# Kernel tuning notes

Measured on AMD Instinct MI355X. Metric: run time of the kernel, lower is better.

## Reference

```python
import jax, jax.numpy as jnp
import numpy as np

# Static config (matches init_kwargs / docstring example)
SHAPES = ((100, 100), (50, 50), (25, 25), (13, 13))  # (H, W) per level
L, P, NH, HD, E, F = 4, 4, 8, 32, 256, 1024
NUM_LAYERS = 6
EPS = 1e-5
NUM_KEYS = sum(h * w for h, w in SHAPES)  # 13294


def _ln(x, g, b):
    m = jnp.mean(x, -1, keepdims=True)
    v = jnp.var(x, -1, keepdims=True)
    return (x - m) * jax.lax.rsqrt(v + EPS) * g + b


def _ms_deform_attn(value, loc, aw):
    # value: (B,N,NH,HD)  loc: (B,N,NH,L,P,2) normalized  aw: (B,N,NH,L,P)
    B, N = value.shape[:2]
    out = jnp.zeros((B, NH, N, HD), value.dtype)
    start = 0
    for lvl, (h, w) in enumerate(SHAPES):
        v = value[:, start:start + h * w].transpose(0, 2, 1, 3)  # (B,NH,hw,HD)
        start += h * w
        # grid_sample align_corners=False pixel coords
        x = loc[:, :, :, lvl, :, 0] * w - 0.5  # (B,N,NH,P)
        y = loc[:, :, :, lvl, :, 1] * h - 0.5
        x0 = jnp.floor(x); y0 = jnp.floor(y)
        lx = x - x0; ly = y - y0
        x0 = x0.astype(jnp.int32); y0 = y0.astype(jnp.int32)

        def gather(yi, xi):
            valid = ((xi >= 0) & (xi < w) & (yi >= 0) & (yi < h)).astype(value.dtype)
            idx = jnp.clip(yi, 0, h - 1) * w + jnp.clip(xi, 0, w - 1)  # (B,N,NH,P)
            idx = idx.transpose(0, 2, 1, 3).reshape(B, NH, N * P, 1)
            got = jnp.take_along_axis(v, idx, axis=2).reshape(B, NH, N, P, HD)
            return got * valid.transpose(0, 2, 1, 3)[..., None]

        def wgt(a):  # (B,N,NH,P) -> (B,NH,N,P,1)
            return a.transpose(0, 2, 1, 3)[..., None]

        samp = (gather(y0, x0) * wgt((1 - lx) * (1 - ly))
                + gather(y0, x0 + 1) * wgt(lx * (1 - ly))
                + gather(y0 + 1, x0) * wgt((1 - lx) * ly)
                + gather(y0 + 1, x0 + 1) * wgt(lx * ly))  # (B,NH,N,P,HD)
        out = out + jnp.sum(samp * wgt(aw[:, :, :, lvl]), axis=3)
    return out.transpose(0, 2, 1, 3).reshape(B, N, NH * HD)


def _layer(x, ref, Woff, boff, Waw, baw, Wv, bv, Wo, bo, ln1_g, ln1_b, Wf1, bf1, Wf2, bf2, ln2_g, ln2_b):
    B, N, _ = x.shape
    v = (x @ Wv + bv).reshape(B, N, NH, HD)
    off = (x @ Woff + boff).reshape(B, N, NH, L, P, 2)
    aw = jax.nn.softmax((x @ Waw + baw).reshape(B, N, NH, L * P), -1).reshape(B, N, NH, L, P)
    normalizer = jnp.asarray([[w, h] for (h, w) in SHAPES], x.dtype)  # (L,2) in (x,y)=(W,H)
    loc = ref[:, :, None, :, None, :] + off / normalizer[None, None, None, :, None, :]
    attn = _ms_deform_attn(v, loc, aw) @ Wo + bo
    x = _ln(x + attn, ln1_g, ln1_b)
    f = jax.nn.relu(x @ Wf1 + bf1) @ Wf2 + bf2
    return _ln(x + f, ln2_g, ln2_b)


def setup_inputs() -> dict:
    key = jax.random.key(0)
    ks = jax.random.split(key, 10)
    s = 0.02
    return {
        "src": jax.random.normal(ks[0], (2, NUM_KEYS, E), jnp.float32),
        "reference_points": jax.random.uniform(ks[1], (2, NUM_KEYS, L, 2), jnp.float32),
        "spatial_shapes": jnp.asarray(SHAPES, jnp.int32),
        "level_start_index": jnp.asarray([0, 10000, 12500, 13125], jnp.int32),
        "Woff": jax.random.normal(ks[2], (E, NH * L * P * 2), jnp.float32) * s,
        "boff": jnp.zeros((NH * L * P * 2,), jnp.float32),
        "Waw": jax.random.normal(ks[3], (E, NH * L * P), jnp.float32) * s,
        "baw": jnp.zeros((NH * L * P,), jnp.float32),
        "Wv": jax.random.normal(ks[4], (E, E), jnp.float32) * s,
        "bv": jnp.zeros((E,), jnp.float32),
        "Wo": jax.random.normal(ks[5], (E, E), jnp.float32) * s,
        "bo": jnp.zeros((E,), jnp.float32),
        "ln1_g": jnp.ones((E,), jnp.float32),
        "ln1_b": jnp.zeros((E,), jnp.float32),
        "Wf1": jax.random.normal(ks[6], (E, F), jnp.float32) * s,
        "bf1": jnp.zeros((F,), jnp.float32),
        "Wf2": jax.random.normal(ks[7], (F, E), jnp.float32) * s,
        "bf2": jnp.zeros((E,), jnp.float32),
        "ln2_g": jnp.ones((E,), jnp.float32),
        "ln2_b": jnp.zeros((E,), jnp.float32),
    }


def reference(src, reference_points, spatial_shapes, level_start_index, Woff, boff, Waw, baw, Wv, bv, Wo, bo, ln1_g, ln1_b, Wf1, bf1, Wf2, bf2, ln2_g, ln2_b):
    # NOTE: the torch encoder reuses the SAME layer object num_layers times,
    # so parameters are shared across all 6 layers.
    x = src
    for _ in range(NUM_LAYERS):
        x = _layer(x, reference_points, Woff, boff, Waw, baw, Wv, bv, Wo, bo,
                   ln1_g, ln1_b, Wf1, bf1, Wf2, bf2, ln2_g, ln2_b)
    return x
```

## Files before the change

### kernel.cpp

```cpp
#include <hip/hip_runtime.h>
#include <hip/hip_bf16.h>
#include <math.h>

#define NKEYS 13294
#define BATCH 2
#define MROWS (BATCH * NKEYS)
#define EDIM  256
#define FDIM  1024
#define EPSV  1e-5f

typedef __bf16 bf16x8 __attribute__((ext_vector_type(8)));
typedef float  f32x4  __attribute__((ext_vector_type(4)));
typedef float  f32x2  __attribute__((ext_vector_type(2)));

__device__ __forceinline__ void async16(const void* g, void* l) {
    __builtin_amdgcn_global_load_lds(
        (const __attribute__((address_space(1))) void*)g,
        (__attribute__((address_space(3))) void*)l, 16, 0, 0);
}

template<int MODE>
__global__ __launch_bounds__(256, 4) void gemm_mfma_k(
    const __hip_bfloat16* __restrict__ A, const __hip_bfloat16* __restrict__ WT,
    const float* __restrict__ bias, __hip_bfloat16* __restrict__ Cout,
    int M, int N, int K,
    __hip_bfloat16* __restrict__ o_vb, __hip_bfloat16* __restrict__ o_off,
    __hip_bfloat16* __restrict__ o_aw)
{
    constexpr int BM = 128, BN = 128, BKc = 32;
    constexpr int SMX = (BM + BN) * BKc;
    __shared__ __hip_bfloat16 smem[2 * SMX];

    const int gx = gridDim.x, nb = gx * gridDim.y;
    int bxi = blockIdx.x, byi = blockIdx.y;
    if ((nb & 7) == 0) {
        const int id   = byi * gx + bxi;
        const int tile = (id & 7) * (nb >> 3) + (id >> 3);
        bxi = tile % gx; byi = tile / gx;
    }
    const int bm = byi * BM;
    const int bn = bxi * BN;

    const int tid  = threadIdx.x;
    const int lane = tid & 63;
    const int w    = tid >> 6;
    const int wr   = w >> 1, wc = w & 1;
    const int l15  = lane & 15, quad = lane >> 4;

    const int gRow = tid >> 2;
    const int kc8  = (tid & 3) * 8;
    const __hip_bfloat16* gsrc[4];
    int ldsoff[4];
    #pragma unroll
    for (int rr = 0; rr < 4; ++rr) {
        const int gr = gRow + 64 * rr;
        if (gr < BM) {
            int ar = bm + gr; if (ar >= M) ar = M - 1;
            gsrc[rr] = A + (size_t)ar * K + kc8;
        } else {
            gsrc[rr] = WT + (size_t)(bn + gr - BM) * K + kc8;
        }
        ldsoff[rr] = gr * BKc + kc8;
    }

    f32x4 acc[4][4];
    #pragma unroll
    for (int i = 0; i < 4; ++i)
        #pragma unroll
        for (int j = 0; j < 4; ++j) acc[i][j] = (f32x4)0.f;

    const int T = K / BKc;
    #pragma unroll
    for (int rr = 0; rr < 4; ++rr) async16(gsrc[rr], smem + ldsoff[rr]);

    for (int it = 0; it < T; ++it) {
        __syncthreads();
        if (it + 1 < T) {
            const int nxt = ((it + 1) & 1) * SMX;
            const int ko  = (it + 1) * BKc;
            #pragma unroll
            for (int rr = 0; rr < 4; ++rr) async16(gsrc[rr] + ko, smem + nxt + ldsoff[rr]);
        }
        const __hip_bfloat16* sA = smem + (it & 1) * SMX;
        const __hip_bfloat16* sB = sA + BM * BKc;

        bf16x8 a[4], b[4];
        #pragma unroll
        for (int mt = 0; mt < 4; ++mt)
            a[mt] = *(const bf16x8*)&sA[(wr * 64 + mt * 16 + l15) * BKc + quad * 8];
        #pragma unroll
        for (int nt = 0; nt < 4; ++nt)
            b[nt] = *(const bf16x8*)&sB[(wc * 64 + nt * 16 + l15) * BKc + quad * 8];
        #pragma unroll
        for (int mt = 0; mt < 4; ++mt)
            #pragma unroll
            for (int nt = 0; nt < 4; ++nt)
                acc[mt][nt] = __builtin_amdgcn_mfma_f32_16x16x32_bf16(
                    a[mt], b[nt], acc[mt][nt], 0, 0, 0);
    }

    #pragma unroll
    for (int mt = 0; mt < 4; ++mt) {
        #pragma unroll
        for (int nt = 0; nt < 4; ++nt) {
            const int col = bn + wc * 64 + nt * 16 + l15;
            const float bz = bias[col];
            #pragma unroll
            for (int r = 0; r < 4; ++r) {
                const int row = bm + wr * 64 + mt * 16 + quad * 4 + r;
                if (row >= M) continue;
                float vv = acc[mt][nt][r] + bz;
                if (MODE == 1) {
                    if (col < 256) {
                        const int b = (row >= NKEYS) ? 1 : 0;
                        const int h = col >> 5, d = col & 31;
                        o_vb[((size_t)(b * 7 + h) * NKEYS + row) * 32 + d] = __float2bfloat16(vv);
                    } else if (col < 512) {
                        o_off[(size_t)row * 256 + (col - 256)] = __float2bfloat16(vv);
                    } else {
                        o_aw[(size_t)row * 128 + (col - 512)] = __float2bfloat16(vv);
                    }
                } else {
                    if (MODE == 3) vv = fmaxf(vv, 0.f);
                    Cout[(size_t)row * N + col] = __float2bfloat16(vv);
                }
            }
        }
    }
}

template<int FINAL>
__global__ __launch_bounds__(256, 2) void gemm_ln_k(
    const __hip_bfloat16* __restrict__ A, const __hip_bfloat16* __restrict__ WT,
    const float* __restrict__ bias, const __hip_bfloat16* __restrict__ xres,
    const float* __restrict__ g, const float* __restrict__ bta,
    float* __restrict__ xfout, __hip_bfloat16* __restrict__ xbout,
    int M, int K)
{
    constexpr int BM = 64, BN = 256, BKc = 32;
    constexpr int ROWS = BM + BN;
    constexpr int SMX = ROWS * BKc;
    __shared__ __hip_bfloat16 smem[2 * SMX];

    const int tid  = threadIdx.x;
    const int bm   = blockIdx.x * BM;
    const int lane = tid & 63;
    const int w    = tid >> 6;
    const int l15  = lane & 15, quad = lane >> 4;

    const int gRow = tid >> 2;
    const int kc8  = (tid & 3) * 8;
    const __hip_bfloat16* gsrc[5];
    int ldsoff[5];
    #pragma unroll
    for (int rr = 0; rr < 5; ++rr) {
        const int gr = gRow + 64 * rr;
        if (gr < BM) {
            int ar = bm + gr; if (ar >= M) ar = M - 1;
            gsrc[rr] = A + (size_t)ar * K + kc8;
        } else {
            gsrc[rr] = WT + (size_t)(gr - BM) * K + kc8;
        }
        ldsoff[rr] = gr * BKc + kc8;
    }

    f32x4 acc[4][4];
    #pragma unroll
    for (int i = 0; i < 4; ++i)
        #pragma unroll
        for (int j = 0; j < 4; ++j) acc[i][j] = (f32x4)0.f;

    const int T = K / BKc;
    #pragma unroll
    for (int rr = 0; rr < 5; ++rr) async16(gsrc[rr], smem + ldsoff[rr]);

    for (int it = 0; it < T; ++it) {
        __syncthreads();
        if (it + 1 < T) {
            const int nxt = ((it + 1) & 1) * SMX;
            const int ko  = (it + 1) * BKc;
            #pragma unroll
            for (int rr = 0; rr < 5; ++rr) async16(gsrc[rr] + ko, smem + nxt + ldsoff[rr]);
        }
        const __hip_bfloat16* sA = smem + (it & 1) * SMX;
        const __hip_bfloat16* sB = sA + BM * BKc;

        bf16x8 a[4], b[4];
        #pragma unroll
        for (int mt = 0; mt < 4; ++mt)
            a[mt] = *(const bf16x8*)&sA[(mt * 16 + l15) * BKc + quad * 8];
        #pragma unroll
        for (int nt = 0; nt < 4; ++nt)
            b[nt] = *(const bf16x8*)&sB[(w * 64 + nt * 16 + l15) * BKc + quad * 8];
        #pragma unroll
        for (int mt = 0; mt < 4; ++mt)
            #pragma unroll
            for (int nt = 0; nt < 4; ++nt)
                acc[mt][nt] = __builtin_amdgcn_mfma_f32_16x16x32_bf16(
                    a[mt], b[nt], acc[mt][nt], 0, 0, 0);
    }

    const int colb = w * 64;
    float bz[4], gz[4], bb[4];
    #pragma unroll
    for (int nt = 0; nt < 4; ++nt) {
        const int col = colb + nt * 16 + l15;
        bz[nt] = bias[col]; gz[nt] = g[col]; bb[nt] = bta[col];
    }
    #pragma unroll
    for (int mt = 0; mt < 4; ++mt)
        #pragma unroll
        for (int r = 0; r < 4; ++r) {
            int row = bm + mt * 16 + quad * 4 + r;
            if (row >= M) row = M - 1;
            #pragma unroll
            for (int nt = 0; nt < 4; ++nt)
                acc[mt][nt][r] += bz[nt] + __bfloat162float(
                    xres[(size_t)row * 256 + colb + nt * 16 + l15]);
        }

    __syncthreads();
    float* stats = (float*)smem;
    #pragma unroll
    for (int mt = 0; mt < 4; ++mt)
        #pragma unroll
        for (int r = 0; r < 4; ++r) {
            float s = 0.f, sq = 0.f;
            #pragma unroll
            for (int nt = 0; nt < 4; ++nt) {
                const float v = acc[mt][nt][r];
                s += v; sq += v * v;
            }
            #pragma unroll
            for (int m = 1; m < 16; m <<= 1) {
                s  += __shfl_xor(s,  m, 64);
                sq += __shfl_xor(sq, m, 64);
            }
            if (l15 == 0) {
                const int rl = mt * 16 + quad * 4 + r;
                stats[(w * 64 + rl) * 2 + 0] = s;
                stats[(w * 64 + rl) * 2 + 1] = sq;
            }
        }
    __syncthreads();

    #pragma unroll
    for (int mt = 0; mt < 4; ++mt)
        #pragma unroll
        for (int r = 0; r < 4; ++r) {
            const int rl  = mt * 16 + quad * 4 + r;
            const int row = bm + rl;
            float s  = stats[rl * 2]          + stats[(64 + rl) * 2]
                     + stats[(128 + rl) * 2]  + stats[(192 + rl) * 2];
            float sq = stats[rl * 2 + 1]      + stats[(64 + rl) * 2 + 1]
                     + stats[(128 + rl) * 2 + 1] + stats[(192 + rl) * 2 + 1];
            const float mean = s * (1.f / 256.f);
            const float var  = sq * (1.f / 256.f) - mean * mean;
            const float rstd = rsqrtf(var + EPSV);
            if (row < M) {
                #pragma unroll
                for (int nt = 0; nt < 4; ++nt) {
                    const int col = colb + nt * 16 + l15;
                    const float v = (acc[mt][nt][r] - mean) * rstd * gz[nt] + bb[nt];
                    xbout[(size_t)row * 256 + col] = __float2bfloat16(v);
                    if (FINAL) xfout[(size_t)row * 256 + col] = v;
                }
            }
        }
}

__global__ void convert_wt_k(const float* __restrict__ W, __hip_bfloat16* __restrict__ WT,
                             int K, int N, int rowOff)
{
    const int idx = blockIdx.x * 256 + threadIdx.x;
    if (idx >= K * N) return;
    const int k = idx / N, n = idx % N;
    WT[(size_t)(rowOff + n) * K + k] = __float2bfloat16(W[idx]);
}

__global__ void pack_bias_k(const float* __restrict__ bv, const float* __restrict__ boff,
                            const float* __restrict__ baw, float* __restrict__ dst)
{
    const int i = blockIdx.x * 256 + threadIdx.x;
    if (i < 256) dst[i] = bv[i];
    else if (i < 512) dst[i] = boff[i - 256];
    else if (i < 640) dst[i] = baw[i - 512];
}

__global__ void convert_src_k(const float* __restrict__ src, __hip_bfloat16* __restrict__ xb)
{
    const int i = blockIdx.x * 256 + threadIdx.x;
    const float4 v = ((const float4*)src)[i];
    xb[i * 4 + 0] = __float2bfloat16(v.x);
    xb[i * 4 + 1] = __float2bfloat16(v.y);
    xb[i * 4 + 2] = __float2bfloat16(v.z);
    xb[i * 4 + 3] = __float2bfloat16(v.w);
}

__global__ __launch_bounds__(256) void sample_k(
    const __hip_bfloat16* __restrict__ v_bf,
    const __hip_bfloat16* __restrict__ offb,
    const __hip_bfloat16* __restrict__ awb,
    const float* __restrict__ ref,
    __hip_bfloat16* __restrict__ out)
{
    __shared__ alignas(16) float sw[272][4];
    __shared__ alignas(16) int   sa[272][4];
    const int t  = threadIdx.x;
    const int q0 = blockIdx.x * 2;
    const int qi = t >> 7, h = (t >> 4) & 7;

    {
        const int i = t & 15;
        const int q = q0 + qi;
        const int l = i >> 2;
        const float logit = __bfloat162float(awb[(size_t)q * 128 + h * 16 + i]);
        float mx = logit;
        #pragma unroll
        for (int m = 1; m < 16; m <<= 1) mx = fmaxf(mx, __shfl_xor(mx, m, 64));
        const float e = __expf(logit - mx);
        float s = e;
        #pragma unroll
        for (int m = 1; m < 16; m <<= 1) s += __shfl_xor(s, m, 64);
        const float aw = e / s;

        const int ww = (l == 0) ? 100 : (l == 1) ? 50 : (l == 2) ? 25 : 13;
        const int ls = (l == 0) ? 0 : (l == 1) ? 10000 : (l == 2) ? 12500 : 13125;
        const int b  = (q >= NKEYS) ? 1 : 0;
        const int slab = (b * 8 + h) * NKEYS + ls;

        const __hip_bfloat162 ofp = *(const __hip_bfloat162*)&offb[(size_t)q * 256 + h * 32 + i * 2];
        const float2 rf = *(const float2*)&ref[(size_t)q * 8 + l * 2];
        const float x = rf.x * (float)ww + __bfloat162float(ofp.x) - 0.5f;
        const float y = rf.y * (float)ww + __bfloat162float(ofp.y) - 0.5f;
        const float x0f = floorf(x), y0f = floorf(y);
        const float lx = x - x0f, ly = y - y0f;
        const int x0 = (int)x0f, y0 = (int)y0f;
        const bool x0ok = (x0 >= 0) & (x0 < ww);
        const bool x1ok = (x0 + 1 >= 0) & (x0 + 1 < ww);
        const bool y0ok = (y0 >= 0) & (y0 < ww);
        const bool y1ok = (y0 + 1 >= 0) & (y0 + 1 < ww);

        float w00 = (1.f - lx) * (1.f - ly) * aw;
        float w01 = lx * (1.f - ly) * aw;
        float w10 = (1.f - lx) * ly * aw;
        float w11 = lx * ly * aw;
        int a00 = slab + y0 * ww + x0;
        int a01 = a00 + 1;
        int a10 = a00 + ww;
        int a11 = a10 + 1;
        if (!(y0ok & x0ok)) { w00 = 0.f; a00 = 0; }
        if (!(y0ok & x1ok)) { w01 = 0.f; a01 = 0; }
        if (!(y1ok & x0ok)) { w10 = 0.f; a10 = 0; }
        if (!(y1ok & x1ok)) { w11 = 0.f; a11 = 0; }

        const int idx = (qi * 8 + h) * 17 + i;
        sw[idx][0] = w00; sw[idx][1] = w01; sw[idx][2] = w10; sw[idx][3] = w11;
        sa[idx][0] = a00 * 64; sa[idx][1] = a01 * 64;
        sa[idx][2] = a10 * 64; sa[idx][3] = a11 * 64;
    }
    __syncthreads();

    const int d2 = t & 15;
    const unsigned d4 = d2 * 4;
    const char* vb = (const char*)v_bf;
    const int ebase = (qi * 8 + h) * 17;
    f32x2 acc = (f32x2)0.f;
    #pragma unroll
    for (int i = 0; i < 16; ++i) {
        const f32x4 wv = *(const f32x4*)sw[ebase + i];
        const int4  av = *(const int4*)sa[ebase + i];
        const unsigned p0 = *(const unsigned*)(vb + ((unsigned)av.x + d4));
        const unsigned p1 = *(const unsigned*)(vb + ((unsigned)av.y + d4));
        const unsigned p2 = *(const unsigned*)(vb + ((unsigned)av.z + d4));
        const unsigned p3 = *(const unsigned*)(vb + ((unsigned)av.w + d4));
        f32x2 v;
        v[0] = __uint_as_float(p0 << 16); v[1] = __uint_as_float(p0 & 0xffff0000u);
        acc += (f32x2)(wv[0]) * v;
        v[0] = __uint_as_float(p1 << 16); v[1] = __uint_as_float(p1 & 0xffff0000u);
        acc += (f32x2)(wv[1]) * v;
        v[0] = __uint_as_float(p2 << 16); v[1] = __uint_as_float(p2 & 0xffff0000u);
        acc += (f32x2)(wv[2]) * v;
        v[0] = __uint_as_float(p3 << 16); v[1] = __uint_as_float(p3 & 0xffff0000u);
        acc += (f32x2)(wv[3]) * v;
    }
    __hip_bfloat162 ov;
    ov.x = __float2bfloat16(acc[0]);
    ov.y = __float2bfloat16(acc[1]);
    *(__hip_bfloat162*)&out[(size_t)(q0 + qi) * 256 + h * 32 + d2 * 2] = ov;
}

extern "C" void kernel_launch(void* const* d_in, const int* in_sizes, int n_in,
                              void* d_out, int out_size, void* d_ws, size_t ws_size,
                              hipStream_t stream)
{
    const float* src  = (const float*)d_in[0];
    const float* ref  = (const float*)d_in[1];
    const float* Woff = (const float*)d_in[4];
    const float* boff = (const float*)d_in[5];
    const float* Waw  = (const float*)d_in[6];
    const float* baw  = (const float*)d_in[7];
    const float* Wv   = (const float*)d_in[8];
    const float* bv   = (const float*)d_in[9];
    const float* Wo   = (const float*)d_in[10];
    const float* bo   = (const float*)d_in[11];
    const float* ln1g = (const float*)d_in[12];
    const float* ln1b = (const float*)d_in[13];
    const float* Wf1  = (const float*)d_in[14];
    const float* bf1  = (const float*)d_in[15];
    const float* Wf2  = (const float*)d_in[16];
    const float* bf2  = (const float*)d_in[17];
    const float* ln2g = (const float*)d_in[18];
    const float* ln2b = (const float*)d_in[19];

    float* x = (float*)d_out;

    float* ws = (float*)d_ws;
    float* bias1 = ws;
    __hip_bfloat16* v_bf  = (__hip_bfloat16*)(bias1 + 640);
    __hip_bfloat16* offb  = v_bf  + (size_t)MROWS * 256;
    __hip_bfloat16* awb   = offb  + (size_t)MROWS * 256;
    __hip_bfloat16* xb    = awb   + (size_t)MROWS * 128;
    __hip_bfloat16* attnb = xb    + (size_t)MROWS * 256;
    __hip_bfloat16* hb    = attnb + (size_t)MROWS * 256;
    __hip_bfloat16* WT1   = hb    + (size_t)MROWS * 1024;
    __hip_bfloat16* WTo   = WT1   + 640 * 256;
    __hip_bfloat16* WTf1  = WTo   + 256 * 256;
    __hip_bfloat16* WTf2  = WTf1  + 1024 * 256;

    convert_wt_k<<<(256 * 256 + 255) / 256, 256, 0, stream>>>(Wv,   WT1,  256, 256,   0);
    convert_wt_k<<<(256 * 256 + 255) / 256, 256, 0, stream>>>(Woff, WT1,  256, 256, 256);
    convert_wt_k<<<(256 * 128 + 255) / 256, 256, 0, stream>>>(Waw,  WT1,  256, 128, 512);
    convert_wt_k<<<(256 * 256 + 255) / 256, 256, 0, stream>>>(Wo,   WTo,  256, 256,   0);
    convert_wt_k<<<(256 * 1024 + 255) / 256, 256, 0, stream>>>(Wf1, WTf1, 256, 1024,  0);
    convert_wt_k<<<(1024 * 256 + 255) / 256, 256, 0, stream>>>(Wf2, WTf2, 1024, 256,  0);
    pack_bias_k<<<3, 256, 0, stream>>>(bv, boff, baw, bias1);
    convert_src_k<<<(MROWS * 64 + 255) / 256, 256, 0, stream>>>(src, xb);

    const int gy  = (MROWS + 127) / 128;
    const int gln = (MROWS + 63) / 64;
    for (int layer = 0; layer < 6; ++layer) {
        gemm_mfma_k<1><<<dim3(640 / 128, gy), 256, 0, stream>>>(
            xb, WT1, bias1, nullptr, MROWS, 640, 256, v_bf, offb, awb);
        sample_k<<<MROWS / 2, 256, 0, stream>>>(v_bf, offb, awb, ref, attnb);
        gemm_ln_k<0><<<gln, 256, 0, stream>>>(
            attnb, WTo, bo, xb, ln1g, ln1b, nullptr, xb, MROWS, 256);
        gemm_mfma_k<3><<<dim3(1024 / 128, gy), 256, 0, stream>>>(
            xb, WTf1, bf1, hb, MROWS, 1024, 256, nullptr, nullptr, nullptr);
        if (layer < 5)
            gemm_ln_k<0><<<gln, 256, 0, stream>>>(
                hb, WTf2, bf2, xb, ln2g, ln2b, nullptr, xb, MROWS, 1024);
        else
            gemm_ln_k<1><<<gln, 256, 0, stream>>>(
                hb, WTf2, bf2, xb, ln2g, ln2b, x, xb, MROWS, 1024);
    }
}
```

Baseline: 1.090 ms.

## Restructure deformable sampling to 8 queries per block with 16-byte gathers

The sampling kernel now handles 8 queries per block instead of 2, with 4 threads per (query, head) each covering 8 channels through 16-byte vector loads, replacing 16 threads doing 4-byte loads. The setup phase has each thread compute 4 sampling points, using vectorized logit and offset loads and a 4-lane softmax reduction. The aim is fewer, wider memory transactions and less per-thread setup overhead. In exchange, per-thread register use and LDS size grow, and a bounds guard is added for the final partial block.

```diff
diff --git a/kernel.cpp b/kernel.cpp
--- a/kernel.cpp
+++ b/kernel.cpp
@@ -12,6 +12,7 @@
 typedef __bf16 bf16x8 __attribute__((ext_vector_type(8)));
 typedef float  f32x4  __attribute__((ext_vector_type(4)));
 typedef float  f32x2  __attribute__((ext_vector_type(2)));
+typedef unsigned short u16x8 __attribute__((ext_vector_type(8)));
 
 __device__ __forceinline__ void async16(const void* g, void* l) {
     __builtin_amdgcn_global_load_lds(
@@ -297,97 +298,120 @@
     xb[i * 4 + 3] = __float2bfloat16(v.w);
 }
 
-__global__ __launch_bounds__(256) void sample_k(
+__global__ __launch_bounds__(256, 4) void sample_k(
     const __hip_bfloat16* __restrict__ v_bf,
     const __hip_bfloat16* __restrict__ offb,
     const __hip_bfloat16* __restrict__ awb,
     const float* __restrict__ ref,
     __hip_bfloat16* __restrict__ out)
 {
-    __shared__ alignas(16) float sw[272][4];
-    __shared__ alignas(16) int   sa[272][4];
+    __shared__ alignas(16) float sw[1088][4];
+    __shared__ alignas(16) int   sa[1088][4];
     const int t  = threadIdx.x;
-    const int q0 = blockIdx.x * 2;
-    const int qi = t >> 7, h = (t >> 4) & 7;
+    const int q0 = blockIdx.x * 8;
+    const int g  = t >> 2;
+    const int qi = g >> 3;
+    const int h  = g & 7;
+    const int q  = q0 + qi;
+    const int qc = (q < MROWS) ? q : (MROWS - 1);
 
     {
-        const int i = t & 15;
-        const int q = q0 + qi;
-        const int l = i >> 2;
-        const float logit = __bfloat162float(awb[(size_t)q * 128 + h * 16 + i]);
-        float mx = logit;
-        #pragma unroll
-        for (int m = 1; m < 16; m <<= 1) mx = fmaxf(mx, __shfl_xor(mx, m, 64));
-        const float e = __expf(logit - mx);
-        float s = e;
-        #pragma unroll
-        for (int m = 1; m < 16; m <<= 1) s += __shfl_xor(s, m, 64);
-        const float aw = e / s;
-
-        const int ww = (l == 0) ? 100 : (l == 1) ? 50 : (l == 2) ? 25 : 13;
-        const int ls = (l == 0) ? 0 : (l == 1) ? 10000 : (l == 2) ? 12500 : 13125;
-        const int b  = (q >= NKEYS) ? 1 : 0;
+        const int j = t & 3;
+        const ushort4 lg4 = *(const ushort4*)&awb[(size_t)qc * 128 + h * 16 + j * 4];
+        float lg[4];
+        lg[0] = __uint_as_float((unsigned)lg4.x << 16);
+        lg[1] = __uint_as_float((unsigned)lg4.y << 16);
+        lg[2] = __uint_as_float((unsigned)lg4.z << 16);
+        lg[3] = __uint_as_float((unsigned)lg4.w << 16);
+        float mx = fmaxf(fmaxf(lg[0], lg[1]), fmaxf(lg[2], lg[3]));
+        mx = fmaxf(mx, __shfl_xor(mx, 1, 64));
+        mx = fmaxf(mx, __shfl_xor(mx, 2, 64));
+        float e[4];
+        e[0] = __expf(lg[0] - mx); e[1] = __expf(lg[1] - mx);
+        e[2] = __expf(lg[2] - mx); e[3] = __expf(lg[3] - mx);
+        float s = e[0] + e[1] + e[2] + e[3];
+        s += __shfl_xor(s, 1, 64);
+        s += __shfl_xor(s, 2, 64);
+        const float rs = 1.f / s;
+
+        const int ww = (j == 0) ? 100 : (j == 1) ? 50 : (j == 2) ? 25 : 13;
+        const int ls = (j == 0) ? 0 : (j == 1) ? 10000 : (j == 2) ? 12500 : 13125;
+        const int b  = (qc >= NKEYS) ? 1 : 0;
         const int slab = (b * 8 + h) * NKEYS + ls;
-
-        const __hip_bfloat162 ofp = *(const __hip_bfloat162*)&offb[(size_t)q * 256 + h * 32 + i * 2];
-        const float2 rf = *(const float2*)&ref[(size_t)q * 8 + l * 2];
-        const float x = rf.x * (float)ww + __bfloat162float(ofp.x) - 0.5f;
-        const float y = rf.y * (float)ww + __bfloat162float(ofp.y) - 0.5f;
-        const float x0f = floorf(x), y0f = floorf(y);
-        const float lx = x - x0f, ly = y - y0f;
-        const int x0 = (int)x0f, y0 = (int)y0f;
-        const bool x0ok = (x0 >= 0) & (x0 < ww);
-        const bool x1ok = (x0 + 1 >= 0) & (x0 + 1 < ww);
-        const bool y0ok = (y0 >= 0) & (y0 < ww);
-        const bool y1ok = (y0 + 1 >= 0) & (y0 + 1 < ww);
-
-        float w00 = (1.f - lx) * (1.f - ly) * aw;
-        float w01 = lx * (1.f - ly) * aw;
-        float w10 = (1.f - lx) * ly * aw;
-        float w11 = lx * ly * aw;
-        int a00 = slab + y0 * ww + x0;
-        int a01 = a00 + 1;
-        int a10 = a00 + ww;
-        int a11 = a10 + 1;
-        if (!(y0ok & x0ok)) { w00 = 0.f; a00 = 0; }
-        if (!(y0ok & x1ok)) { w01 = 0.f; a01 = 0; }
-        if (!(y1ok & x0ok)) { w10 = 0.f; a10 = 0; }
-        if (!(y1ok & x1ok)) { w11 = 0.f; a11 = 0; }
-
-        const int idx = (qi * 8 + h) * 17 + i;
-        sw[idx][0] = w00; sw[idx][1] = w01; sw[idx][2] = w10; sw[idx][3] = w11;
-        sa[idx][0] = a00 * 64; sa[idx][1] = a01 * 64;
-        sa[idx][2] = a10 * 64; sa[idx][3] = a11 * 64;
+        const float2 rf = *(const float2*)&ref[(size_t)qc * 8 + j * 2];
+        const u16x8 of = *(const u16x8*)&offb[(size_t)qc * 256 + h * 32 + j * 8];
+        const float fw = (float)ww;
+
+        #pragma unroll
+        for (int k = 0; k < 4; ++k) {
+            const float aw = e[k] * rs;
+            const float x = rf.x * fw + __uint_as_float((unsigned)of[2 * k]     << 16) - 0.5f;
+            const float y = rf.y * fw + __uint_as_float((unsigned)of[2 * k + 1] << 16) - 0.5f;
+            const float x0f = floorf(x), y0f = floorf(y);
+            const float lx = x - x0f, ly = y - y0f;
+            const int x0 = (int)x0f, y0 = (int)y0f;
+            const bool x0ok = (x0 >= 0) & (x0 < ww);
+            const bool x1ok = (x0 + 1 >= 0) & (x0 + 1 < ww);
+            const bool y0ok = (y0 >= 0) & (y0 < ww);
+            const bool y1ok = (y0 + 1 >= 0) & (y0 + 1 < ww);
+
+            float w00 = (1.f - lx) * (1.f - ly) * aw;
+            float w01 = lx * (1.f - ly) * aw;
+            float w10 = (1.f - lx) * ly * aw;
+            float w11 = lx * ly * aw;
+            int a00 = slab + y0 * ww + x0;
+            int a01 = a00 + 1;
+            int a10 = a00 + ww;
+            int a11 = a10 + 1;
+            if (!(y0ok & x0ok)) { w00 = 0.f; a00 = 0; }
+            if (!(y0ok & x1ok)) { w01 = 0.f; a01 = 0; }
+            if (!(y1ok & x0ok)) { w10 = 0.f; a10 = 0; }
+            if (!(y1ok & x1ok)) { w11 = 0.f; a11 = 0; }
+
+            const int idx = g * 17 + j * 4 + k;
+            sw[idx][0] = w00; sw[idx][1] = w01; sw[idx][2] = w10; sw[idx][3] = w11;
+            sa[idx][0] = a00 * 64; sa[idx][1] = a01 * 64;
+            sa[idx][2] = a10 * 64; sa[idx][3] = a11 * 64;
+        }
     }
     __syncthreads();
 
-    const int d2 = t & 15;
-    const unsigned d4 = d2 * 4;
+    const int d8 = t & 3;
+    const unsigned dof = (unsigned)d8 * 16;
     const char* vb = (const char*)v_bf;
-    const int ebase = (qi * 8 + h) * 17;
-    f32x2 acc = (f32x2)0.f;
+    f32x4 aA = (f32x4)0.f, aB = (f32x4)0.f;
+
+    #define CORNER(AV, W) {                                               \
+        const uint4 p = *(const uint4*)(vb + ((unsigned)(AV) + dof));     \
+        aA[0] += (W) * __uint_as_float(p.x << 16);                        \
+        aA[1] += (W) * __uint_as_float(p.x & 0xffff0000u);                \
+        aA[2] += (W) * __uint_as_float(p.y << 16);                        \
+        aA[3] += (W) * __uint_as_float(p.y & 0xffff0000u);                \
+        aB[0] += (W) * __uint_as_float(p.z << 16);                        \
+        aB[1] += (W) * __uint_as_float(p.z & 0xffff0000u);                \
+        aB[2] += (W) * __uint_as_float(p.w << 16);                        \
+        aB[3] += (W) * __uint_as_float(p.w & 0xffff0000u);                \
+    }
+
     #pragma unroll
     for (int i = 0; i < 16; ++i) {
-        const f32x4 wv = *(const f32x4*)sw[ebase + i];
-        const int4  av = *(const int4*)sa[ebase + i];
-        const unsigned p0 = *(const unsigned*)(vb + ((unsigned)av.x + d4));
-        const unsigned p1 = *(const unsigned*)(vb + ((unsigned)av.y + d4));
-        const unsigned p2 = *(const unsigned*)(vb + ((unsigned)av.z + d4));
-        const unsigned p3 = *(const unsigned*)(vb + ((unsigned)av.w + d4));
-        f32x2 v;
-        v[0] = __uint_as_float(p0 << 16); v[1] = __uint_as_float(p0 & 0xffff0000u);
-        acc += (f32x2)(wv[0]) * v;
-        v[0] = __uint_as_float(p1 << 16); v[1] = __uint_as_float(p1 & 0xffff0000u);
-        acc += (f32x2)(wv[1]) * v;
-        v[0] = __uint_as_float(p2 << 16); v[1] = __uint_as_float(p2 & 0xffff0000u);
-        acc += (f32x2)(wv[2]) * v;
-        v[0] = __uint_as_float(p3 << 16); v[1] = __uint_as_float(p3 & 0xffff0000u);
-        acc += (f32x2)(wv[3]) * v;
-    }
-    __hip_bfloat162 ov;
-    ov.x = __float2bfloat16(acc[0]);
-    ov.y = __float2bfloat16(acc[1]);
-    *(__hip_bfloat162*)&out[(size_t)(q0 + qi) * 256 + h * 32 + d2 * 2] = ov;
+        const f32x4 wv = *(const f32x4*)sw[g * 17 + i];
+        const int4  av = *(const int4*)sa[g * 17 + i];
+        CORNER(av.x, wv[0]);
+        CORNER(av.y, wv[1]);
+        CORNER(av.z, wv[2]);
+        CORNER(av.w, wv[3]);
+    }
+    #undef CORNER
+
+    if (q < MROWS) {
+        union { uint4 u; __hip_bfloat16 b[8]; } o;
+        o.b[0] = __float2bfloat16(aA[0]); o.b[1] = __float2bfloat16(aA[1]);
+        o.b[2] = __float2bfloat16(aA[2]); o.b[3] = __float2bfloat16(aA[3]);
+        o.b[4] = __float2bfloat16(aB[0]); o.b[5] = __float2bfloat16(aB[1]);
+        o.b[6] = __float2bfloat16(aB[2]); o.b[7] = __float2bfloat16(aB[3]);
+        *(uint4*)&out[(size_t)q * 256 + h * 32 + d8 * 8] = o.u;
+    }
 }
 
 extern "C" void kernel_launch(void* const* d_in, const int* in_sizes, int n_in,
@@ -442,7 +466,7 @@
     for (int layer = 0; layer < 6; ++layer) {
         gemm_mfma_k<1><<<dim3(640 / 128, gy), 256, 0, stream>>>(
             xb, WT1, bias1, nullptr, MROWS, 640, 256, v_bf, offb, awb);
-        sample_k<<<MROWS / 2, 256, 0, stream>>>(v_bf, offb, awb, ref, attnb);
+        sample_k<<<(MROWS + 7) / 8, 256, 0, stream>>>(v_bf, offb, awb, ref, attnb);
         gemm_ln_k<0><<<gln, 256, 0, stream>>>(
             attnb, WTo, bo, xb, ln1g, ln1b, nullptr, xb, MROWS, 256);
         gemm_mfma_k<3><<<dim3(1024 / 128, gy), 256, 0, stream>>>(
```

After: 1.281 ms. +17.5%, slower.
